# Optimization experiments

Measured on AMD Instinct MI355X. Metric: run time of the kernel, lower is better.

## Reference

```python
import jax, jax.numpy as jnp
import numpy as np

D_MODEL = 1024


def setup_inputs() -> dict:
    key = jax.random.key(0)
    kx, kq, kk, kv = jax.random.split(key, 4)
    x = jax.random.normal(kx, (4, 2048, D_MODEL), dtype=jnp.float32)
    s = 1.0 / np.sqrt(D_MODEL)
    # torch nn.Linear weight is [out, in]; y = x @ W.T
    Wq = jax.random.normal(kq, (D_MODEL, D_MODEL), dtype=jnp.float32) * s
    Wk = jax.random.normal(kk, (D_MODEL, D_MODEL), dtype=jnp.float32) * s
    Wv = jax.random.normal(kv, (D_MODEL, D_MODEL), dtype=jnp.float32) * s
    return {"x": x, "Wq": Wq, "Wk": Wk, "Wv": Wv}


def reference(x, Wq, Wk, Wv):
    # Linear projections (no bias): [b, s, d]
    Q = jnp.einsum("bsd,ed->bse", x, Wq)
    K = jnp.einsum("bsd,ed->bse", x, Wk)
    V = jnp.einsum("bsd,ed->bse", x, Wv)
    d_k = Q.shape[-1]
    scores = jnp.einsum("bqd,bkd->bqk", Q, K) / jnp.sqrt(jnp.asarray(d_k, Q.dtype))
    weights = jax.nn.softmax(scores, axis=-1)
    return jnp.einsum("bqk,bkd->bqd", weights, V)
```

## Files before the change

kernel.cpp:

```cpp
#include <hip/hip_runtime.h>
#include <hip/hip_bf16.h>

using bf16 = __hip_bfloat16;
typedef __attribute__((ext_vector_type(8))) short short8;
typedef __attribute__((ext_vector_type(16))) float f32x16;

__global__ __launch_bounds__(256) void cast_all(const float* __restrict__ x,
                                                const float* __restrict__ Wq,
                                                const float* __restrict__ Wk,
                                                const float* __restrict__ Wv,
                                                bf16* __restrict__ xb, bf16* __restrict__ Wb) {
  const int b = blockIdx.x;
  const float* src;
  bf16* dst;
  if (b < 8192) {
    src = x + (size_t)b * 1024;
    dst = xb + (size_t)b * 1024;
  } else if (b < 9216) {
    src = Wq + (size_t)(b - 8192) * 1024;
    dst = Wb + (size_t)(b - 8192) * 1024;
  } else if (b < 10240) {
    src = Wk + (size_t)(b - 9216) * 1024;
    dst = Wb + (size_t)(b - 8192) * 1024;
  } else {
    src = Wv + (size_t)(b - 10240) * 1024;
    dst = Wb + (size_t)(b - 8192) * 1024;
  }
  const int i = threadIdx.x * 4;
  const float4 f = *(const float4*)(src + i);
  bf16 h[4];
  h[0] = __float2bfloat16(f.x);
  h[1] = __float2bfloat16(f.y);
  h[2] = __float2bfloat16(f.z);
  h[3] = __float2bfloat16(f.w);
  *(uint2*)(dst + i) = *(const uint2*)h;
}

template <class Epi>
__device__ __forceinline__ void gemm_nt(const bf16* __restrict__ A, const bf16* __restrict__ B,
                                        int lda, int ldb, int K, int m0, int n0, Epi epi) {
  constexpr int BK = 32;
  constexpr int CPR = 4;
  constexpr int SH = 2;
  constexpr int N_INSTR = 2;
  constexpr int SLOT = 128 * BK * 2 * 2;
  __shared__ char smem[2 * SLOT];
  const int t = threadIdx.x;
  const int lane = t & 63;
  const int wave = t >> 6;
  const int wm = (wave >> 1) * 64;
  const int wn = (wave & 1) * 64;

  f32x16 acc[2][2];
#pragma unroll
  for (int i = 0; i < 2; ++i)
#pragma unroll
    for (int j = 0; j < 2; ++j)
#pragma unroll
      for (int r = 0; r < 16; ++r) acc[i][j][r] = 0.f;

  const bf16* gA[N_INSTR];
  const bf16* gB[N_INSTR];
#pragma unroll
  for (int j = 0; j < N_INSTR; ++j) {
    const int slot = j * 256 + t;
    const int row = slot >> SH;
    const int f = (row + (row >> SH)) & (CPR - 1);
    const int c = ((slot & (CPR - 1)) ^ f) << 3;
    gA[j] = A + (size_t)(m0 + row) * lda + c;
    gB[j] = B + (size_t)(n0 + row) * ldb + c;
  }

  const int rl = lane & 31;
  const int grp = lane >> 5;

  auto stage = [&](int kt) {
    char* base = smem + (kt & 1) * SLOT;
    bf16* As = (bf16*)base;
    bf16* Bs = (bf16*)(base + 128 * BK * 2);
    const int k0 = kt * BK;
#pragma unroll
    for (int j = 0; j < N_INSTR; ++j) {
      __builtin_amdgcn_global_load_lds(
          (const __attribute__((address_space(1))) unsigned int*)(gA[j] + k0),
          (__attribute__((address_space(3))) unsigned int*)(As + (j * 256 + wave * 64) * 8), 16, 0, 0);
      __builtin_amdgcn_global_load_lds(
          (const __attribute__((address_space(1))) unsigned int*)(gB[j] + k0),
          (__attribute__((address_space(3))) unsigned int*)(Bs + (j * 256 + wave * 64) * 8), 16, 0, 0);
    }
  };

  const int NT = K >> 5;

  stage(0);
  asm volatile("s_waitcnt vmcnt(0)" ::: "memory");
  __builtin_amdgcn_s_barrier();
  __builtin_amdgcn_sched_barrier(0);

  for (int kt = 0; kt < NT; ++kt) {
    const char* base = smem + (kt & 1) * SLOT;
    const bf16* As = (const bf16*)base;
    const bf16* Bs = (const bf16*)(base + 128 * BK * 2);

    short8 af[2][2], bv[2][2];
#pragma unroll
    for (int ks = 0; ks < 2; ++ks) {
      const int kb = ks * 2 + grp;
#pragma unroll
      for (int mt = 0; mt < 2; ++mt) {
        const int rowa = wm + mt * 32 + rl;
        const int fa = (rowa + (rowa >> SH)) & (CPR - 1);
        af[ks][mt] = *(const short8*)(As + rowa * BK + ((kb ^ fa) << 3));
        const int rowb = wn + mt * 32 + rl;
        const int fb = (rowb + (rowb >> SH)) & (CPR - 1);
        bv[ks][mt] = *(const short8*)(Bs + rowb * BK + ((kb ^ fb) << 3));
      }
    }
    if (kt + 1 < NT) stage(kt + 1);

    __builtin_amdgcn_sched_barrier(0);
    asm volatile("s_waitcnt lgkmcnt(0)" ::: "memory");
    __builtin_amdgcn_sched_barrier(0);
    __builtin_amdgcn_s_setprio(1);
#pragma unroll
    for (int ks = 0; ks < 2; ++ks)
#pragma unroll
      for (int mt = 0; mt < 2; ++mt)
#pragma unroll
        for (int nt = 0; nt < 2; ++nt)
          acc[mt][nt] = __builtin_amdgcn_mfma_f32_32x32x16_bf16(af[ks][mt], bv[ks][nt],
                                                                acc[mt][nt], 0, 0, 0);
    __builtin_amdgcn_s_setprio(0);
    __builtin_amdgcn_sched_barrier(0);
    asm volatile("s_waitcnt vmcnt(0)" ::: "memory");
    __builtin_amdgcn_s_barrier();
    __builtin_amdgcn_sched_barrier(0);
  }
  __syncthreads();

  epi(acc, m0, n0, wm, wn, lane, wave, smem);
}

__device__ __forceinline__ int c_row(int reg, int lane) {
  return (reg & 3) + 8 * (reg >> 2) + 4 * (lane >> 5);
}

template <class F>
__device__ __forceinline__ void for_each_c(const f32x16 (&acc)[2][2], int wm, int wn, int lane,
                                           F f) {
  const int rl = lane & 31;
#pragma unroll
  for (int mt = 0; mt < 2; ++mt)
#pragma unroll
    for (int nt = 0; nt < 2; ++nt)
#pragma unroll
      for (int reg = 0; reg < 16; ++reg)
        f(wm + mt * 32 + c_row(reg, lane), wn + nt * 32 + rl, acc[mt][nt][reg]);
}

__global__ __launch_bounds__(256, 4) void proj_kernel(const bf16* __restrict__ xb,
                                                      const bf16* __restrict__ Wb,
                                                      bf16* __restrict__ Qb,
                                                      bf16* __restrict__ Kb,
                                                      bf16* __restrict__ Vt) {
  const int id = blockIdx.y * 24 + blockIdx.x;
  const int g = id & 7, s = id >> 3;
  const int m0 = (g * 8 + (s & 7)) * 128;
  const int n0 = (s >> 3) * 128;
  gemm_nt(xb, Wb, 1024, 1024, 1024, m0, n0,
          [=](const f32x16 (&acc)[2][2], int m0, int n0, int wm, int wn, int lane, int wave,
              char* smem) {
    if (n0 < 2048) {
      bf16* dst = (n0 < 1024) ? Qb : Kb;
      const int nb = (n0 < 1024) ? n0 : (n0 - 1024);
      for_each_c(acc, wm, wn, lane, [&](int m, int n, float v) {
        dst[(size_t)(m0 + m) * 1024 + nb + n] = __float2bfloat16(v);
      });
    } else {
      bf16* T = (bf16*)(smem) + wave * 2304;
      const int rl = lane & 31;
      const int g4 = 4 * (lane >> 5);
      const int mbase = m0 + wm;
      const int bb = mbase >> 11;
      const int sbase = mbase & 2047;
      const int nvbase = n0 - 2048 + wn;
#pragma unroll
      for (int p = 0; p < 2; ++p) {
#pragma unroll
        for (int mt = 0; mt < 2; ++mt)
#pragma unroll
          for (int q = 0; q < 4; ++q) {
            bf16 h4[4];
#pragma unroll
            for (int r = 0; r < 4; ++r) h4[r] = __float2bfloat16(acc[mt][p][4 * q + r]);
            *(uint2*)(T + rl * 72 + mt * 32 + 8 * q + g4) = *(const uint2*)h4;
          }
        asm volatile("s_waitcnt lgkmcnt(0)" ::: "memory");
#pragma unroll
        for (int i = 0; i < 4; ++i) {
          const int nl = i * 8 + (lane >> 3);
          const int ml = (lane & 7) * 8;
          const short8 val = *(const short8*)(T + nl * 72 + ml);
          *(short8*)(Vt + ((size_t)bb * 1024 + nvbase + p * 32 + nl) * 2048 + sbase + ml) = val;
        }
        asm volatile("s_waitcnt lgkmcnt(0)" ::: "memory");
      }
    }
  });
}

__global__ __launch_bounds__(256, 4) void qk_exp_kernel(const bf16* __restrict__ Qb,
                                                        const bf16* __restrict__ Kb,
                                                        bf16* __restrict__ E,
                                                        float* __restrict__ Lpart) {
  const int z = blockIdx.z;
  const int id2 = blockIdx.y * 16 + blockIdx.x;
  const int g = id2 & 7, s = id2 >> 3;
  const int m0 = ((g & 3) * 4 + (s & 3)) * 128;
  const int n0 = ((g >> 2) * 8 + (s >> 2)) * 128;
  const bf16* A = Qb + (size_t)z * 2048 * 1024;
  const bf16* B = Kb + (size_t)z * 2048 * 1024;
  bf16* Ez = E + (size_t)z * 2048 * 2048;
  float* Lz = Lpart + (size_t)z * 16 * 2048;
  gemm_nt(A, B, 1024, 1024, 1024, m0, n0,
          [=](const f32x16 (&acc)[2][2], int m0, int n0, int wm, int wn, int lane, int wave,
              char* smem) {
    float* Lp = (float*)smem;
    const int rl = lane & 31;
#pragma unroll
    for (int mt = 0; mt < 2; ++mt)
#pragma unroll
      for (int reg = 0; reg < 16; ++reg) {
        const int mr = wm + mt * 32 + c_row(reg, lane);
        float s2 = 0.f;
#pragma unroll
        for (int nt = 0; nt < 2; ++nt) {
          const float e = __expf(acc[mt][nt][reg] * 0.03125f);
          Ez[(size_t)(m0 + mr) * 2048 + n0 + wn + nt * 32 + rl] = __float2bfloat16(e);
          s2 += e;
        }
        s2 += __shfl_xor(s2, 1, 64);
        s2 += __shfl_xor(s2, 2, 64);
        s2 += __shfl_xor(s2, 4, 64);
        s2 += __shfl_xor(s2, 8, 64);
        s2 += __shfl_xor(s2, 16, 64);
        if (rl == 0) Lp[mr * 2 + (wave & 1)] = s2;
      }
    __syncthreads();
    const int t = threadIdx.x;
    if (t < 128) Lz[(n0 >> 7) * 2048 + m0 + t] = Lp[t * 2 + 0] + Lp[t * 2 + 1];
  });
}

__global__ __launch_bounds__(256, 4) void pv_kernel(const bf16* __restrict__ E,
                                                    const bf16* __restrict__ Vt,
                                                    const float* __restrict__ Lpart,
                                                    float* __restrict__ out) {
  const int z = blockIdx.z;
  const int id2 = blockIdx.y * 8 + blockIdx.x;
  const int g = id2 & 7, s = id2 >> 3;
  const int m0 = ((g & 3) * 4 + (s & 3)) * 128;
  const int n0 = ((g >> 2) * 4 + (s >> 2)) * 128;
  const bf16* A = E + (size_t)z * 2048 * 2048;
  const bf16* B = Vt + (size_t)z * 1024 * 2048;
  const float* Lz = Lpart + (size_t)z * 16 * 2048;
  float* oz = out + (size_t)z * 2048 * 1024;
  gemm_nt(A, B, 2048, 2048, 2048, m0, n0,
          [=](const f32x16 (&acc)[2][2], int m0, int n0, int wm, int wn, int lane, int wave,
              char* smem) {
    float* Lsm = (float*)smem;
    const int t = threadIdx.x;
    if (t < 128) {
      float s2 = 0.f;
#pragma unroll
      for (int i = 0; i < 16; ++i) s2 += Lz[(size_t)i * 2048 + m0 + t];
      Lsm[t] = 1.f / s2;
    }
    __syncthreads();
    const int rl = lane & 31;
#pragma unroll
    for (int mt = 0; mt < 2; ++mt)
#pragma unroll
      for (int reg = 0; reg < 16; ++reg) {
        const int ml = wm + mt * 32 + c_row(reg, lane);
        const float il = Lsm[ml];
#pragma unroll
        for (int nt = 0; nt < 2; ++nt)
          oz[(size_t)(m0 + ml) * 1024 + n0 + wn + nt * 32 + rl] = acc[mt][nt][reg] * il;
      }
  });
}

extern "C" void kernel_launch(void* const* d_in, const int* in_sizes, int n_in,
                              void* d_out, int out_size, void* d_ws, size_t ws_size,
                              hipStream_t stream) {
  const float* x = (const float*)d_in[0];
  const float* Wq = (const float*)d_in[1];
  const float* Wk = (const float*)d_in[2];
  const float* Wv = (const float*)d_in[3];
  float* out = (float*)d_out;

  char* w = (char*)d_ws;
  bf16* xb = (bf16*)w; w += (size_t)8192 * 1024 * 2;
  bf16* Wb = (bf16*)w; w += (size_t)3072 * 1024 * 2;
  bf16* Qb = (bf16*)w; w += (size_t)8192 * 1024 * 2;
  bf16* Kb = (bf16*)w; w += (size_t)8192 * 1024 * 2;
  bf16* Vt = (bf16*)w; w += (size_t)8192 * 1024 * 2;
  bf16* E  = (bf16*)w; w += (size_t)4 * 2048 * 2048 * 2;
  float* Lpart = (float*)w; w += (size_t)4 * 16 * 2048 * 4;

  cast_all<<<11264, 256, 0, stream>>>(x, Wq, Wk, Wv, xb, Wb);

  proj_kernel<<<dim3(24, 64), 256, 0, stream>>>(xb, Wb, Qb, Kb, Vt);

  qk_exp_kernel<<<dim3(16, 16, 4), 256, 0, stream>>>(Qb, Kb, E, Lpart);

  pv_kernel<<<dim3(8, 16, 4), 256, 0, stream>>>(E, Vt, Lpart, out);
}
```

Before: 248.5 us.

## Widen GEMM tiles to 128x256 with 8 waves and triple-buffered LDS pipeline

The shared GEMM core now uses 512-thread blocks (8 waves in a 2x4 layout) that compute 128x256 output tiles, so each A tile is reused across twice as many columns and the grid has half as many blocks. The LDS double buffer becomes a three-slot ring with prefetch two k-steps ahead and partial vmcnt waits, which keeps more loads in flight per iteration. The partial softmax denominators shrink from 16 to 8 column chunks per row. The cost is more LDS per block (72KB), which may lower occupancy, and the proj epilogue now relies on the new wave layout and smem size.

Result: faster. 229.5 us (-7.7%).

```diff
diff --git a/kernel.cpp b/kernel.cpp
--- a/kernel.cpp
+++ b/kernel.cpp
@@ -39,68 +39,70 @@
 template <class Epi>
 __device__ __forceinline__ void gemm_nt(const bf16* __restrict__ A, const bf16* __restrict__ B,
                                         int lda, int ldb, int K, int m0, int n0, Epi epi) {
-  constexpr int BK = 32;
-  constexpr int CPR = 4;
-  constexpr int SH = 2;
-  constexpr int N_INSTR = 2;
-  constexpr int SLOT = 128 * BK * 2 * 2;
-  __shared__ char smem[2 * SLOT];
+  constexpr int SLOT = 24576;
+  __shared__ char smem[3 * SLOT];
   const int t = threadIdx.x;
   const int lane = t & 63;
   const int wave = t >> 6;
-  const int wm = (wave >> 1) * 64;
-  const int wn = (wave & 1) * 64;
-
-  f32x16 acc[2][2];
-#pragma unroll
-  for (int i = 0; i < 2; ++i)
-#pragma unroll
-    for (int j = 0; j < 2; ++j)
-#pragma unroll
-      for (int r = 0; r < 16; ++r) acc[i][j][r] = 0.f;
-
-  const bf16* gA[N_INSTR];
-  const bf16* gB[N_INSTR];
-#pragma unroll
-  for (int j = 0; j < N_INSTR; ++j) {
-    const int slot = j * 256 + t;
-    const int row = slot >> SH;
-    const int f = (row + (row >> SH)) & (CPR - 1);
-    const int c = ((slot & (CPR - 1)) ^ f) << 3;
-    gA[j] = A + (size_t)(m0 + row) * lda + c;
-    gB[j] = B + (size_t)(n0 + row) * ldb + c;
-  }
-
+  const int wm = (wave >> 2) * 64;
+  const int wn = (wave & 3) * 64;
   const int rl = lane & 31;
   const int grp = lane >> 5;
 
-  auto stage = [&](int kt) {
-    char* base = smem + (kt & 1) * SLOT;
+  f32x16 acc[2][2];
+#pragma unroll
+  for (int i = 0; i < 2; ++i)
+#pragma unroll
+    for (int j = 0; j < 2; ++j)
+#pragma unroll
+      for (int r = 0; r < 16; ++r) acc[i][j][r] = 0.f;
+
+  const bf16* gA0;
+  {
+    const int row = t >> 2;
+    const int f = (row + (row >> 2)) & 3;
+    gA0 = A + (size_t)(m0 + row) * lda + ((((t & 3) ^ f)) << 3);
+  }
+  const bf16* gB[2];
+#pragma unroll
+  for (int j = 0; j < 2; ++j) {
+    const int s = j * 512 + t;
+    const int row = s >> 2;
+    const int f = (row + (row >> 2)) & 3;
+    gB[j] = B + (size_t)(n0 + row) * ldb + ((((s & 3) ^ f)) << 3);
+  }
+
+  auto stage = [&](int kt, int slot) {
+    char* base = smem + slot * SLOT;
     bf16* As = (bf16*)base;
-    bf16* Bs = (bf16*)(base + 128 * BK * 2);
-    const int k0 = kt * BK;
-#pragma unroll
-    for (int j = 0; j < N_INSTR; ++j) {
-      __builtin_amdgcn_global_load_lds(
-          (const __attribute__((address_space(1))) unsigned int*)(gA[j] + k0),
-          (__attribute__((address_space(3))) unsigned int*)(As + (j * 256 + wave * 64) * 8), 16, 0, 0);
+    bf16* Bs = (bf16*)(base + 8192);
+    const int k0 = kt * 32;
+    __builtin_amdgcn_global_load_lds(
+        (const __attribute__((address_space(1))) unsigned int*)(gA0 + k0),
+        (__attribute__((address_space(3))) unsigned int*)(As + wave * 512), 16, 0, 0);
+#pragma unroll
+    for (int j = 0; j < 2; ++j)
       __builtin_amdgcn_global_load_lds(
           (const __attribute__((address_space(1))) unsigned int*)(gB[j] + k0),
-          (__attribute__((address_space(3))) unsigned int*)(Bs + (j * 256 + wave * 64) * 8), 16, 0, 0);
-    }
+          (__attribute__((address_space(3))) unsigned int*)(Bs + (j * 512 + wave * 64) * 8), 16, 0, 0);
   };
 
   const int NT = K >> 5;
 
-  stage(0);
-  asm volatile("s_waitcnt vmcnt(0)" ::: "memory");
+  stage(0, 0);
+  stage(1, 1);
+  asm volatile("s_waitcnt vmcnt(3)" ::: "memory");
   __builtin_amdgcn_s_barrier();
   __builtin_amdgcn_sched_barrier(0);
 
+  int sr = 0;
+  int ss = 2;
   for (int kt = 0; kt < NT; ++kt) {
-    const char* base = smem + (kt & 1) * SLOT;
+    const char* base = smem + sr * SLOT;
     const bf16* As = (const bf16*)base;
-    const bf16* Bs = (const bf16*)(base + 128 * BK * 2);
+    const bf16* Bs = (const bf16*)(base + 8192);
+
+    if (kt + 2 < NT) stage(kt + 2, ss);
 
     short8 af[2][2], bv[2][2];
 #pragma unroll
@@ -109,15 +111,13 @@
 #pragma unroll
       for (int mt = 0; mt < 2; ++mt) {
         const int rowa = wm + mt * 32 + rl;
-        const int fa = (rowa + (rowa >> SH)) & (CPR - 1);
-        af[ks][mt] = *(const short8*)(As + rowa * BK + ((kb ^ fa) << 3));
+        const int fa = (rowa + (rowa >> 2)) & 3;
+        af[ks][mt] = *(const short8*)(As + rowa * 32 + ((kb ^ fa) << 3));
         const int rowb = wn + mt * 32 + rl;
-        const int fb = (rowb + (rowb >> SH)) & (CPR - 1);
-        bv[ks][mt] = *(const short8*)(Bs + rowb * BK + ((kb ^ fb) << 3));
+        const int fb = (rowb + (rowb >> 2)) & 3;
+        bv[ks][mt] = *(const short8*)(Bs + rowb * 32 + ((kb ^ fb) << 3));
       }
     }
-    if (kt + 1 < NT) stage(kt + 1);
-
     __builtin_amdgcn_sched_barrier(0);
     asm volatile("s_waitcnt lgkmcnt(0)" ::: "memory");
     __builtin_amdgcn_sched_barrier(0);
@@ -132,9 +132,17 @@
                                                                 acc[mt][nt], 0, 0, 0);
     __builtin_amdgcn_s_setprio(0);
     __builtin_amdgcn_sched_barrier(0);
-    asm volatile("s_waitcnt vmcnt(0)" ::: "memory");
-    __builtin_amdgcn_s_barrier();
-    __builtin_amdgcn_sched_barrier(0);
+    if (kt + 1 < NT) {
+      if (kt + 2 < NT) {
+        asm volatile("s_waitcnt vmcnt(3)" ::: "memory");
+      } else {
+        asm volatile("s_waitcnt vmcnt(0)" ::: "memory");
+      }
+      __builtin_amdgcn_s_barrier();
+      __builtin_amdgcn_sched_barrier(0);
+    }
+    sr = (sr == 2) ? 0 : sr + 1;
+    ss = (ss == 2) ? 0 : ss + 1;
   }
   __syncthreads();
 
@@ -158,15 +166,15 @@
         f(wm + mt * 32 + c_row(reg, lane), wn + nt * 32 + rl, acc[mt][nt][reg]);
 }
 
-__global__ __launch_bounds__(256, 4) void proj_kernel(const bf16* __restrict__ xb,
+__global__ __launch_bounds__(512, 4) void proj_kernel(const bf16* __restrict__ xb,
                                                       const bf16* __restrict__ Wb,
                                                       bf16* __restrict__ Qb,
                                                       bf16* __restrict__ Kb,
                                                       bf16* __restrict__ Vt) {
-  const int id = blockIdx.y * 24 + blockIdx.x;
+  const int id = blockIdx.y * 12 + blockIdx.x;
   const int g = id & 7, s = id >> 3;
   const int m0 = (g * 8 + (s & 7)) * 128;
-  const int n0 = (s >> 3) * 128;
+  const int n0 = (s >> 3) * 256;
   gemm_nt(xb, Wb, 1024, 1024, 1024, m0, n0,
           [=](const f32x16 (&acc)[2][2], int m0, int n0, int wm, int wn, int lane, int wave,
               char* smem) {
@@ -209,19 +217,19 @@
   });
 }
 
-__global__ __launch_bounds__(256, 4) void qk_exp_kernel(const bf16* __restrict__ Qb,
+__global__ __launch_bounds__(512, 4) void qk_exp_kernel(const bf16* __restrict__ Qb,
                                                         const bf16* __restrict__ Kb,
                                                         bf16* __restrict__ E,
                                                         float* __restrict__ Lpart) {
-  const int z = blockIdx.z;
-  const int id2 = blockIdx.y * 16 + blockIdx.x;
+  const int z = blockIdx.y;
+  const int id2 = blockIdx.x;
   const int g = id2 & 7, s = id2 >> 3;
   const int m0 = ((g & 3) * 4 + (s & 3)) * 128;
-  const int n0 = ((g >> 2) * 8 + (s >> 2)) * 128;
+  const int n0 = ((g >> 2) * 4 + (s >> 2)) * 256;
   const bf16* A = Qb + (size_t)z * 2048 * 1024;
   const bf16* B = Kb + (size_t)z * 2048 * 1024;
   bf16* Ez = E + (size_t)z * 2048 * 2048;
-  float* Lz = Lpart + (size_t)z * 16 * 2048;
+  float* Lz = Lpart + (size_t)z * 8 * 2048;
   gemm_nt(A, B, 1024, 1024, 1024, m0, n0,
           [=](const f32x16 (&acc)[2][2], int m0, int n0, int wm, int wn, int lane, int wave,
               char* smem) {
@@ -244,26 +252,28 @@
         s2 += __shfl_xor(s2, 4, 64);
         s2 += __shfl_xor(s2, 8, 64);
         s2 += __shfl_xor(s2, 16, 64);
-        if (rl == 0) Lp[mr * 2 + (wave & 1)] = s2;
+        if (rl == 0) Lp[mr * 4 + (wave & 3)] = s2;
       }
     __syncthreads();
     const int t = threadIdx.x;
-    if (t < 128) Lz[(n0 >> 7) * 2048 + m0 + t] = Lp[t * 2 + 0] + Lp[t * 2 + 1];
+    if (t < 128)
+      Lz[(n0 >> 8) * 2048 + m0 + t] =
+          Lp[t * 4 + 0] + Lp[t * 4 + 1] + Lp[t * 4 + 2] + Lp[t * 4 + 3];
   });
 }
 
-__global__ __launch_bounds__(256, 4) void pv_kernel(const bf16* __restrict__ E,
+__global__ __launch_bounds__(512, 4) void pv_kernel(const bf16* __restrict__ E,
                                                     const bf16* __restrict__ Vt,
                                                     const float* __restrict__ Lpart,
                                                     float* __restrict__ out) {
-  const int z = blockIdx.z;
-  const int id2 = blockIdx.y * 8 + blockIdx.x;
+  const int z = blockIdx.y;
+  const int id2 = blockIdx.x;
   const int g = id2 & 7, s = id2 >> 3;
   const int m0 = ((g & 3) * 4 + (s & 3)) * 128;
-  const int n0 = ((g >> 2) * 4 + (s >> 2)) * 128;
+  const int n0 = ((g >> 2) * 2 + (s >> 2)) * 256;
   const bf16* A = E + (size_t)z * 2048 * 2048;
   const bf16* B = Vt + (size_t)z * 1024 * 2048;
-  const float* Lz = Lpart + (size_t)z * 16 * 2048;
+  const float* Lz = Lpart + (size_t)z * 8 * 2048;
   float* oz = out + (size_t)z * 2048 * 1024;
   gemm_nt(A, B, 2048, 2048, 2048, m0, n0,
           [=](const f32x16 (&acc)[2][2], int m0, int n0, int wm, int wn, int lane, int wave,
@@ -273,7 +283,7 @@
     if (t < 128) {
       float s2 = 0.f;
 #pragma unroll
-      for (int i = 0; i < 16; ++i) s2 += Lz[(size_t)i * 2048 + m0 + t];
+      for (int i = 0; i < 8; ++i) s2 += Lz[(size_t)i * 2048 + m0 + t];
       Lsm[t] = 1.f / s2;
     }
     __syncthreads();
@@ -307,13 +317,13 @@
   bf16* Kb = (bf16*)w; w += (size_t)8192 * 1024 * 2;
   bf16* Vt = (bf16*)w; w += (size_t)8192 * 1024 * 2;
   bf16* E  = (bf16*)w; w += (size_t)4 * 2048 * 2048 * 2;
-  float* Lpart = (float*)w; w += (size_t)4 * 16 * 2048 * 4;
+  float* Lpart = (float*)w; w += (size_t)4 * 8 * 2048 * 4;
 
   cast_all<<<11264, 256, 0, stream>>>(x, Wq, Wk, Wv, xb, Wb);
 
-  proj_kernel<<<dim3(24, 64), 256, 0, stream>>>(xb, Wb, Qb, Kb, Vt);
-
-  qk_exp_kernel<<<dim3(16, 16, 4), 256, 0, stream>>>(Qb, Kb, E, Lpart);
-
-  pv_kernel<<<dim3(8, 16, 4), 256, 0, stream>>>(E, Vt, Lpart, out);
-}
+  proj_kernel<<<dim3(12, 64), 512, 0, stream>>>(xb, Wb, Qb, Kb, Vt);
+
+  qk_exp_kernel<<<dim3(128, 4), 512, 0, stream>>>(Qb, Kb, E, Lpart);
+
+  pv_kernel<<<dim3(64, 4), 512, 0, stream>>>(E, Vt, Lpart, out);
+}
```
